# Kernel tuning notes

Measured on AMD Instinct MI355X. Metric: run time of the kernel, lower is better.

The kernel has to match this reference:

```python
import jax, jax.numpy as jnp
import numpy as np

B, S, H, A = 64, 200, 256, 16
CAPS_LAYERS = 3
NEG = -1e9
LN_EPS = 1e-12


def _layernorm(x, g, b):
    mu = jnp.mean(x, axis=-1, keepdims=True)
    var = jnp.mean(jnp.square(x - mu), axis=-1, keepdims=True)
    return (x - mu) / jnp.sqrt(var + LN_EPS) * g + b


def setup_inputs() -> dict:
    key = jax.random.key(0)
    ks = jax.random.split(key, 10)
    s = 0.02  # initializer_range
    return {
        "item_emb": jax.random.normal(ks[0], (B, S, H), jnp.float32),
        "item_seq": jax.random.randint(ks[1], (B, S), 0, 50000),
        "time_seq": jax.random.randint(ks[2], (B, S, 2), 0, 14),
        "W_lin": s * jax.random.normal(ks[3], (H, H), jnp.float32),
        "b_lin": jnp.zeros((H,), jnp.float32),
        "aspect_embs": s * jax.random.normal(ks[4], (A, H), jnp.float32),
        "pos_emb": s * jax.random.normal(ks[5], (S, H), jnp.float32),
        "tdt_emb": s * jax.random.normal(ks[6], (14, H), jnp.float32),
        "tdn_emb": s * jax.random.normal(ks[7], (14, H), jnp.float32),
        "Wa1": s * jax.random.normal(ks[8], (H, H), jnp.float32),
        "ba1": jnp.zeros((H,), jnp.float32),
        "Wa2": s * jax.random.normal(ks[9], (H,), jnp.float32),
        "ba2": jnp.zeros((1,), jnp.float32),
        "ln_g": jnp.ones((H,), jnp.float32),
        "ln_b": jnp.zeros((H,), jnp.float32),
    }


def reference(item_emb, item_seq, time_seq, W_lin, b_lin, aspect_embs,
              pos_emb, tdt_emb, tdn_emb, Wa1, ba1, Wa2, ba2, ln_g, ln_b):
    b, s = item_emb.shape[0], item_emb.shape[1]
    pad = item_seq == 0  # [B,S]

    # ---- TimeAwareAttention (seq_output has a singleton neighbor dim in torch) ----
    td = tdt_emb[time_seq[:, :, 0]] + tdn_emb[time_seq[:, :, 1]]       # [B,S,H]
    tma_in = pos_emb[None, :s] + item_emb + td                          # [B,S,H]
    h = tma_in @ Wa1 + ba1
    h = jnp.where(h >= 0, h, 0.01 * h)                                  # LeakyReLU
    w = h @ Wa2 + ba2[0]                                                # [B,S]
    w = jnp.where(pad, NEG, w)
    tma = jax.nn.softmax(w, axis=-1)                                    # [B,S]

    # ---- gating (eval: clean gates) ----
    gates = jnp.einsum('bsh,ah->bsa', item_emb, aspect_embs)            # [B,S,A]
    idx = jnp.argmax(gates, axis=-1)                                    # topk k=1, [B,S]

    src = jnp.where(pad, 0.0, 1.0)
    counts = jnp.zeros((b, A), jnp.float32).at[jnp.arange(b)[:, None], idx].add(src)
    aspect_mask = counts == 0                                           # [B,A]

    # ---- item transform (dropout = identity in eval) ----
    moe = _layernorm(jnp.tanh(item_emb @ W_lin + b_lin) + item_emb, ln_g, ln_b)  # [B,S,H]

    # ---- capsule routing ----
    bij = gates
    cap = jnp.broadcast_to(aspect_embs[None], (b, A, H))
    for _ in range(CAPS_LAYERS):
        cij = jnp.where(aspect_mask[:, None, :], NEG, bij)
        cij = jax.nn.softmax(cij, axis=-1)
        cij = jnp.where(pad[:, :, None], 0.0, cij)                      # [B,S,A]
        cap = jnp.einsum('bsa,bsh,bs->bah', cij, moe, tma)              # [B,A,H]
        n2 = jnp.sum(jnp.square(cap), axis=-1, keepdims=True)
        cap = n2 / (1.0 + n2) / jnp.sqrt(n2 + 1e-9) * cap               # squash
        bij = bij + jnp.einsum('bsh,bah->bsa', moe, cap)

    # ---- gather activated interests / activation positions ----
    activated = cap[jnp.arange(b)[:, None], idx]                        # [B,S,H]
    seq_pos = jnp.where(pad, 0, jnp.arange(1, s + 1)[None, :]).astype(jnp.float32)
    act_mat = jnp.full((b, s, A), -1.0, jnp.float32)
    act_mat = act_mat.at[jnp.arange(b)[:, None], jnp.arange(s)[None, :], idx].set(seq_pos)
    act_mat = jnp.where(pad[:, :, None], -1.0, act_mat)
    max_pos = jnp.max(act_mat, axis=1)                                  # [B,A]
    aspects_item_idx = jnp.where(max_pos > -1.0, max_pos - 1.0, max_pos)

    gates_sm = jax.nn.softmax(gates, axis=-1)
    return (cap, gates_sm, aspect_mask, activated, aspects_item_idx, idx[:, :, None])
```

## Files before the change

### kernel.cpp

```cpp
#include <hip/hip_runtime.h>

#define B_ 64
#define S_ 200
#define H_ 256
#define A_ 16
#define M_ (B_*S_)
#define NEGV (-1000000000.0f)

typedef unsigned short ushortT;
typedef __attribute__((ext_vector_type(8))) short short8;
typedef __attribute__((ext_vector_type(4))) float f32x4;

__device__ __forceinline__ ushortT bf16u(float f) {
  unsigned int u = __builtin_bit_cast(unsigned int, f);
  unsigned int r = (u + 0x7fffu + ((u >> 16) & 1u)) >> 16;
  return (ushortT)r;
}
__device__ __forceinline__ float bf2f(ushortT u) {
  unsigned int v = ((unsigned int)u) << 16;
  return __builtin_bit_cast(float, v);
}

__global__ __launch_bounds__(256) void prepT_kernel(
    const float* __restrict__ Wa1, const float* __restrict__ W_lin,
    ushortT* __restrict__ Wa1T, ushortT* __restrict__ WlinT)
{
  __shared__ float T[64*65];
  const int blk = blockIdx.x, t = threadIdx.x;
  int wsel = blk >> 4;
  int tile = blk & 15;
  const float* W = wsel ? W_lin : Wa1;
  ushortT* WT = wsel ? WlinT : Wa1T;
  int tr = (tile >> 2) * 64, tc = (tile & 3) * 64;
  #pragma unroll
  for (int p = 0; p < 16; ++p) {
    int r = p*4 + (t >> 6);
    int c = t & 63;
    T[c*65 + r] = W[(tr + r)*H_ + tc + c];
  }
  __syncthreads();
  #pragma unroll
  for (int p = 0; p < 16; ++p) {
    int n = p*4 + (t >> 6);
    int k = t & 63;
    WT[(tc + n)*H_ + tr + k] = bf16u(T[n*65 + k]);
  }
}

__global__ __launch_bounds__(512) void fused_kernel(
    const float* __restrict__ item, const int* __restrict__ iseq,
    const int* __restrict__ tseq, const float* __restrict__ pos,
    const float* __restrict__ tdt, const float* __restrict__ tdn,
    const float* __restrict__ asp,
    const ushortT* __restrict__ Wa1T, const ushortT* __restrict__ WlinT,
    const float* __restrict__ ba1, const float* __restrict__ Wa2,
    const float* __restrict__ ba2, const float* __restrict__ b_lin,
    const float* __restrict__ g_ln, const float* __restrict__ b_ln,
    float* __restrict__ w_out, ushortT* __restrict__ moe_outB,
    float* __restrict__ graw, float* __restrict__ gates_sm,
    float* __restrict__ idxf)
{
  __shared__ __align__(16) ushortT smem[51200];
  __shared__ int sL[64], ttL[64], tnL[64];
  __shared__ float wp[2][64], ln1[2][64], ln2[2][64], mus[64], rss[64];

  const int t = threadIdx.x;
  const int m0 = blockIdx.x * 64;
  const int lane = t & 63, w = t >> 6;
  const int g = w >> 2, wl = w & 3;
  const int wm = wl >> 1, wn = wl & 1;
  const int col = lane & 15;
  const int rg  = lane >> 4;

  if (t < 64) {
    int m = m0 + t;
    sL[t]  = m % S_;
    ttL[t] = tseq[2*m];
    tnL[t] = tseq[2*m+1];
  }
  __syncthreads();

  const int arow = t >> 3;
  const int ac4  = (t & 7) * 4;
  const int nr   = t >> 1;
  const int kh   = (t & 1) * 16;
  const int srow = sL[arow], trow = ttL[arow], nrow = tnL[arow];

  ushortT* const Atma0 = smem;
  ushortT* const Aitm0 = smem + 5120;
  ushortT* const B0b   = smem + 10240;
  ushortT* const B1b   = smem + 30720;

  float4 pi = *(const float4*)&item[(size_t)(m0+arow)*H_ + ac4];
  float4 pp = *(const float4*)&pos[srow*H_ + ac4];
  float4 pt = *(const float4*)&tdt[trow*H_ + ac4];
  float4 pn = *(const float4*)&tdn[nrow*H_ + ac4];
  uint4 b0a = *(const uint4*)&Wa1T[(size_t)nr*H_ + kh];
  uint4 b0b = *(const uint4*)&Wa1T[(size_t)nr*H_ + kh + 8];
  uint4 b1a = *(const uint4*)&WlinT[(size_t)nr*H_ + kh];
  uint4 b1b = *(const uint4*)&WlinT[(size_t)nr*H_ + kh + 8];
  {
    union { ushortT u[4]; uint2 v; } ci, ct;
    ci.u[0] = bf16u(pi.x); ci.u[1] = bf16u(pi.y);
    ci.u[2] = bf16u(pi.z); ci.u[3] = bf16u(pi.w);
    ct.u[0] = bf16u(pi.x + pp.x + pt.x + pn.x);
    ct.u[1] = bf16u(pi.y + pp.y + pt.y + pn.y);
    ct.u[2] = bf16u(pi.z + pp.z + pt.z + pn.z);
    ct.u[3] = bf16u(pi.w + pp.w + pt.w + pn.w);
    *(uint2*)&Aitm0[arow*40 + ac4] = ci.v;
    *(uint2*)&Atma0[arow*40 + ac4] = ct.v;
    *(uint4*)&B0b[nr*40 + kh]     = b0a;
    *(uint4*)&B0b[nr*40 + kh + 8] = b0b;
    *(uint4*)&B1b[nr*40 + kh]     = b1a;
    *(uint4*)&B1b[nr*40 + kh + 8] = b1b;
  }
  __syncthreads();

  f32x4 acc[2][8];
  #pragma unroll
  for (int r = 0; r < 2; ++r)
    #pragma unroll
    for (int q = 0; q < 8; ++q) acc[r][q] = (f32x4){0.f,0.f,0.f,0.f};

  #pragma unroll
  for (int ks = 0; ks < 8; ++ks) {
    if (ks < 7) {
      const int k1 = (ks + 1) * 32;
      pi = *(const float4*)&item[(size_t)(m0+arow)*H_ + k1 + ac4];
      pp = *(const float4*)&pos[srow*H_ + k1 + ac4];
      pt = *(const float4*)&tdt[trow*H_ + k1 + ac4];
      pn = *(const float4*)&tdn[nrow*H_ + k1 + ac4];
      b0a = *(const uint4*)&Wa1T[(size_t)nr*H_ + k1 + kh];
      b0b = *(const uint4*)&Wa1T[(size_t)nr*H_ + k1 + kh + 8];
      b1a = *(const uint4*)&WlinT[(size_t)nr*H_ + k1 + kh];
      b1b = *(const uint4*)&WlinT[(size_t)nr*H_ + k1 + kh + 8];
    }
    {
      const int p = ks & 1;
      const ushortT* Ab = (g ? Aitm0 : Atma0) + p*2560;
      const ushortT* Bb = (g ? B1b : B0b) + p*10240;
      short8 af0 = *(const short8*)&Ab[(wm*32 + col)*40 + rg*8];
      short8 af1 = *(const short8*)&Ab[(wm*32 + 16 + col)*40 + rg*8];
      #pragma unroll
      for (int q = 0; q < 8; ++q) {
        short8 bf = *(const short8*)&Bb[(wn*128 + q*16 + col)*40 + rg*8];
        acc[0][q] = __builtin_amdgcn_mfma_f32_16x16x32_bf16(af0, bf, acc[0][q], 0, 0, 0);
        acc[1][q] = __builtin_amdgcn_mfma_f32_16x16x32_bf16(af1, bf, acc[1][q], 0, 0, 0);
      }
    }
    if (ks < 7) {
      const int p = (ks + 1) & 1;
      union { ushortT u[4]; uint2 v; } ci, ct;
      ci.u[0] = bf16u(pi.x); ci.u[1] = bf16u(pi.y);
      ci.u[2] = bf16u(pi.z); ci.u[3] = bf16u(pi.w);
      ct.u[0] = bf16u(pi.x + pp.x + pt.x + pn.x);
      ct.u[1] = bf16u(pi.y + pp.y + pt.y + pn.y);
      ct.u[2] = bf16u(pi.z + pp.z + pt.z + pn.z);
      ct.u[3] = bf16u(pi.w + pp.w + pt.w + pn.w);
      *(uint2*)&(Aitm0 + p*2560)[arow*40 + ac4] = ci.v;
      *(uint2*)&(Atma0 + p*2560)[arow*40 + ac4] = ct.v;
      ushortT* B0w = B0b + p*10240;
      ushortT* B1w = B1b + p*10240;
      *(uint4*)&B0w[nr*40 + kh]     = b0a;
      *(uint4*)&B0w[nr*40 + kh + 8] = b0b;
      *(uint4*)&B1w[nr*40 + kh]     = b1a;
      *(uint4*)&B1w[nr*40 + kh + 8] = b1b;
    }
    __syncthreads();
  }

  float* aspl = (float*)smem;
  float* gL   = (float*)smem + 4160;
  #pragma unroll
  for (int i = 0; i < 2; ++i) {
    int e = t + 512*i;
    int r = e >> 6, c = e & 63;
    *(float4*)&aspl[r*260 + 4*c] = *(const float4*)&asp[r*H_ + 4*c];
  }

  float glv[8], bbv[8];
  if (g == 0) {
    float bav[8], wav[8];
    #pragma unroll
    for (int q = 0; q < 8; ++q) {
      int n = wn*128 + q*16 + col;
      bav[q] = ba1[n]; wav[q] = Wa2[n];
    }
    #pragma unroll
    for (int r = 0; r < 2; ++r)
      #pragma unroll
      for (int j = 0; j < 4; ++j) {
        float p = 0.f;
        #pragma unroll
        for (int q = 0; q < 8; ++q) {
          float h = acc[r][q][j] + bav[q];
          h = (h >= 0.f) ? h : 0.01f*h;
          p += h * wav[q];
        }
        #pragma unroll
        for (int mk = 1; mk < 16; mk <<= 1) p += __shfl_xor(p, mk);
        if (col == 0) wp[wn][wm*32 + r*16 + rg*4 + j] = p;
      }
  } else {
    float blv[8];
    #pragma unroll
    for (int q = 0; q < 8; ++q) {
      int n = wn*128 + q*16 + col;
      blv[q] = b_lin[n]; glv[q] = g_ln[n]; bbv[q] = b_ln[n];
    }
    #pragma unroll
    for (int r = 0; r < 2; ++r)
      #pragma unroll
      for (int j = 0; j < 4; ++j) {
        int row = wm*32 + r*16 + rg*4 + j;
        float s1 = 0.f, s2 = 0.f;
        #pragma unroll
        for (int q = 0; q < 8; ++q) {
          int n = wn*128 + q*16 + col;
          float vv = tanhf(acc[r][q][j] + blv[q]) + item[(size_t)(m0+row)*H_ + n];
          acc[r][q][j] = vv; s1 += vv; s2 += vv*vv;
        }
        #pragma unroll
        for (int mk = 1; mk < 16; mk <<= 1) {
          s1 += __shfl_xor(s1, mk);
          s2 += __shfl_xor(s2, mk);
        }
        if (col == 0) { ln1[wn][row] = s1; ln2[wn][row] = s2; }
      }
  }
  __syncthreads();
  if (t < 64) {
    int row = t, m = m0 + row;
    w_out[m] = (iseq[m] == 0) ? NEGV : (wp[0][row] + wp[1][row] + ba2[0]);
  } else if (t < 128) {
    int row = t - 64;
    float s1 = ln1[0][row] + ln1[1][row];
    float s2 = ln2[0][row] + ln2[1][row];
    float mu  = s1 * (1.0f/H_);
    float var = s2 * (1.0f/H_) - mu*mu;
    mus[row] = mu;
    rss[row] = 1.0f / sqrtf(fmaxf(var, 0.f) + 1e-12f);
  }
  __syncthreads();
  if (g == 1) {
    #pragma unroll
    for (int r = 0; r < 2; ++r)
      #pragma unroll
      for (int j = 0; j < 4; ++j) {
        int row = wm*32 + r*16 + rg*4 + j;
        int m = m0 + row;
        float mu = mus[row], rs = rss[row];
        #pragma unroll
        for (int q = 0; q < 8; ++q) {
          int n = wn*128 + q*16 + col;
          moe_outB[(size_t)m*H_ + n] = bf16u((acc[r][q][j] - mu)*rs*glv[q] + bbv[q]);
        }
      }
  }

  {
    const int r8 = t >> 3, a2 = (t & 7) * 2;
    const int m = m0 + r8;
    float ga = 0.f, gb = 0.f;
    #pragma unroll 8
    for (int k4 = 0; k4 < 64; ++k4) {
      float4 xv = *(const float4*)&item[(size_t)m*H_ + 4*k4];
      float4 a0 = *(const float4*)&aspl[a2*260 + 4*k4];
      float4 a1 = *(const float4*)&aspl[(a2+1)*260 + 4*k4];
      ga += xv.x*a0.x + xv.y*a0.y + xv.z*a0.z + xv.w*a0.w;
      gb += xv.x*a1.x + xv.y*a1.y + xv.z*a1.z + xv.w*a1.w;
    }
    gL[r8*20 + a2]     = ga;
    gL[r8*20 + a2 + 1] = gb;
  }
  __syncthreads();
  if (t < 64) {
    float row[16];
    #pragma unroll
    for (int a = 0; a < 16; ++a) row[a] = gL[t*20 + a];
    float best = row[0]; int bi = 0;
    #pragma unroll
    for (int a = 1; a < 16; ++a)
      if (row[a] > best) { best = row[a]; bi = a; }
    idxf[m0 + t] = (float)bi;
    float mx = row[0];
    #pragma unroll
    for (int a = 1; a < 16; ++a) mx = fmaxf(mx, row[a]);
    float ex[16], sm = 0.f;
    #pragma unroll
    for (int a = 0; a < 16; ++a) { ex[a] = expf(row[a] - mx); sm += ex[a]; }
    float inv = 1.f / sm;
    #pragma unroll
    for (int q = 0; q < 4; ++q) {
      float4 rv; rv.x = row[4*q]; rv.y = row[4*q+1]; rv.z = row[4*q+2]; rv.w = row[4*q+3];
      *(float4*)&graw[(m0+t)*A_ + 4*q] = rv;
      float4 o; o.x = ex[4*q]*inv; o.y = ex[4*q+1]*inv; o.z = ex[4*q+2]*inv; o.w = ex[4*q+3]*inv;
      *(float4*)&gates_sm[(m0+t)*A_ + 4*q] = o;
    }
  }
}

__device__ __forceinline__ float blk_max(float v, float* red) {
  #pragma unroll
  for (int mk = 32; mk; mk >>= 1) v = fmaxf(v, __shfl_xor(v, mk));
  int t = threadIdx.x;
  if ((t & 63) == 0) red[t >> 6] = v;
  __syncthreads();
  if (t < 64) {
    float x = (t < 16) ? red[t] : -3.0e38f;
    #pragma unroll
    for (int mk = 8; mk; mk >>= 1) x = fmaxf(x, __shfl_xor(x, mk));
    if (t == 0) red[0] = x;
  }
  __syncthreads();
  float r = red[0];
  __syncthreads();
  return r;
}

__device__ __forceinline__ float blk_sum(float v, float* red) {
  #pragma unroll
  for (int mk = 32; mk; mk >>= 1) v += __shfl_xor(v, mk);
  int t = threadIdx.x;
  if ((t & 63) == 0) red[t >> 6] = v;
  __syncthreads();
  if (t < 64) {
    float x = (t < 16) ? red[t] : 0.f;
    #pragma unroll
    for (int mk = 8; mk; mk >>= 1) x += __shfl_xor(x, mk);
    if (t == 0) red[0] = x;
  }
  __syncthreads();
  float r = red[0];
  __syncthreads();
  return r;
}

#define WGSTR 232
#define CBSTR 260
#define CLSTR 252

__global__ __launch_bounds__(1024) void phaseC_kernel(
    const int* __restrict__ iseq, const float* __restrict__ w_in,
    const ushortT* __restrict__ moeB, const float* __restrict__ idxf,
    const float* __restrict__ graw,
    float* __restrict__ cap_out,
    float* __restrict__ mask_out,
    float* __restrict__ aidx_out,
    float* __restrict__ act_out)
{
  __shared__ ushortT moeTr[57344];
  __shared__ ushortT wgtT[16*WGSTR];
  __shared__ ushortT capB[16*CBSTR];
  __shared__ float bij[4032];
  __shared__ float n2p[16*17];
  __shared__ float n2s[16];
  __shared__ float tmaL[S_];
  __shared__ float red[16];
  __shared__ float maskf[A_];
  __shared__ int counts[A_], maxpos[A_];
  __shared__ int idxl[S_];
  __shared__ int padl[S_];

  const int t = threadIdx.x;
  const int b = blockIdx.x;
  const int base = b * S_;
  const int lane = t & 63, w = t >> 6;
  const int la = lane & 15, lg = lane >> 4;

  #pragma unroll
  for (int u = 0; u < 4; ++u) {
    int e = t + 1024*u;
    if (e < 3584) {
      int ht = e & 15, s = e >> 4;
      int ks = s >> 5, s4l = (s >> 2) & 7, sr = s & 3;
      int bp = (s4l & 1) ? 4 + (s4l >> 1) : (s4l >> 1);
      int li = ((ht*7 + ks)*8 + bp)*64 + sr*16;
      if (s < S_) {
        const ushortT* gp = &moeB[((size_t)(base + s))*H_ + ht*16];
        *(uint4*)&moeTr[li]     = *(const uint4*)gp;
        *(uint4*)&moeTr[li + 8] = *(const uint4*)(gp + 8);
      } else {
        uint4 z = {0,0,0,0};
        *(uint4*)&moeTr[li] = z; *(uint4*)&moeTr[li + 8] = z;
      }
    }
  }
  if (t < 512) {
    int a = t >> 5, s = 200 + (t & 31);
    wgtT[a*WGSTR + s] = 0;
  }

  if (t < A_) { counts[t] = 0; maxpos[t] = -1; }
  float wv = -3.0e38f;
  if (t < S_) {
    int s = t;
    padl[s] = (iseq[base+s] == 0) ? 1 : 0;
    idxl[s] = (int)idxf[base+s];
    wv = w_in[base+s];
    #pragma unroll
    for (int q = 0; q < 4; ++q)
      *(float4*)&bij[s*20 + 4*q] = *(const float4*)&graw[(base+s)*A_ + 4*q];
  }
  __syncthreads();

  short8 a2[7];
  {
    unsigned vA = (unsigned)(w*7168 + lane*8);
    #pragma unroll
    for (int ks = 0; ks < 7; ++ks) {
      long long r0, r1;
      asm volatile(
        "ds_read_b64_tr_b16 %0, %2\n\t"
        "ds_read_b64_tr_b16 %1, %2 offset:512\n\t"
        "s_waitcnt lgkmcnt(0)"
        : "=&v"(r0), "=&v"(r1) : "v"(vA + (unsigned)(ks*1024)) : "memory");
      __builtin_amdgcn_sched_barrier(0);
      union { short8 v; long long q[2]; } uu;
      uu.q[0] = r0; uu.q[1] = r1;
      a2[ks] = uu.v;
    }
  }

  if (t < S_ && !padl[t]) {
    atomicAdd(&counts[idxl[t]], 1);
    atomicMax(&maxpos[idxl[t]], t + 1);
  }
  float mxw = blk_max(wv, red);
  float ev = (t < S_) ? expf(wv - mxw) : 0.f;
  float sw = blk_sum(ev, red);
  if (t < S_) tmaL[t] = ev / sw;
  __syncthreads();
  if (t < A_) {
    int c = counts[t];
    float mkv = (c == 0) ? 1.f : 0.f;
    maskf[t] = mkv;
    mask_out[b*A_ + t] = mkv;
    int mp = maxpos[t];
    aidx_out[b*A_ + t] = (mp > 0) ? (float)(mp - 1) : -1.f;
  }
  __syncthreads();

  for (int iter = 0; iter < 3; ++iter) {
    #pragma unroll
    for (int pass = 0; pass < 4; ++pass) {
      int s = pass*64 + (t >> 4);
      int a = t & 15;
      if (s < S_) {
        float v = bij[s*20 + a];
        v = (maskf[a] > 0.5f) ? NEGV : v;
        float mx = v;
        #pragma unroll
        for (int mk = 1; mk < 16; mk <<= 1) mx = fmaxf(mx, __shfl_xor(mx, mk));
        float e = expf(v - mx);
        float sm = e;
        #pragma unroll
        for (int mk = 1; mk < 16; mk <<= 1) sm += __shfl_xor(sm, mk);
        float sc = (padl[s] ? 0.f : tmaL[s]) / sm;
        wgtT[a*WGSTR + s] = bf16u(e*sc);
      }
    }
    __syncthreads();

    f32x4 acc = (f32x4){0.f,0.f,0.f,0.f};
    #pragma unroll
    for (int ks = 0; ks < 7; ++ks) {
      short8 bf = *(const short8*)&wgtT[la*WGSTR + ks*32 + lg*8];
      acc = __builtin_amdgcn_mfma_f32_16x16x32_bf16(a2[ks], bf, acc, 0, 0, 0);
    }
    {
      float n2 = acc[0]*acc[0] + acc[1]*acc[1] + acc[2]*acc[2] + acc[3]*acc[3];
      n2 += __shfl_xor(n2, 16);
      n2 += __shfl_xor(n2, 32);
      if (lane < 16) n2p[w*17 + lane] = n2;
    }
    __syncthreads();
    if (t < 16) {
      float sv = 0.f;
      #pragma unroll
      for (int w2 = 0; w2 < 16; ++w2) sv += n2p[w2*17 + t];
      n2s[t] = sv / (1.f + sv) / sqrtf(sv + 1e-9f);
    }
    __syncthreads();
    {
      float sc = n2s[la];
      if (iter < 2) {
        #pragma unroll
        for (int r = 0; r < 4; ++r)
          capB[la*CBSTR + w*16 + lg*4 + r] = bf16u(acc[r]*sc);
      } else {
        float* capl = bij;
        #pragma unroll
        for (int r = 0; r < 4; ++r)
          capl[la*CLSTR + w*16 + lg*4 + r] = acc[r]*sc;
      }
    }
    __syncthreads();

    if (iter < 2) {
      if (w < 13) {
        int sR = w*16 + la;
        int ksS = sR >> 5, s4l = (sR >> 2) & 7, sr = sR & 3;
        int bp = (s4l & 1) ? 4 + (s4l >> 1) : (s4l >> 1);
        int laneA = ksS*512 + bp*64 + sr*16 + (lg & 1)*8 + (lg >> 1)*3584;
        f32x4 accS = (f32x4){0.f,0.f,0.f,0.f};
        #pragma unroll
        for (int k4 = 0; k4 < 8; ++k4) {
          short8 am = *(const short8*)&moeTr[laneA + k4*7168];
          short8 bc = *(const short8*)&capB[la*CBSTR + k4*32 + lg*8];
          accS = __builtin_amdgcn_mfma_f32_16x16x32_bf16(am, bc, accS, 0, 0, 0);
        }
        int sW = w*16 + lg*4;
        #pragma unroll
        for (int r = 0; r < 4; ++r)
          if (sW + r < S_) bij[(sW + r)*20 + la] += accS[r];
      }
      __syncthreads();
    }
  }

  {
    const float* capl = bij;
    int a = t >> 6, h4 = t & 63;
    float4 v = *(const float4*)&capl[a*CLSTR + 4*h4];
    *(float4*)&cap_out[((size_t)b*A_ + a)*H_ + 4*h4] = v;
    for (int s = t >> 6; s < S_; s += 16) {
      float4 av = *(const float4*)&capl[idxl[s]*CLSTR + 4*h4];
      *(float4*)&act_out[((size_t)base + s)*H_ + 4*h4] = av;
    }
  }
}

extern "C" void kernel_launch(void* const* d_in, const int* in_sizes, int n_in,
                              void* d_out, int out_size, void* d_ws, size_t ws_size,
                              hipStream_t stream) {
  (void)in_sizes; (void)n_in; (void)out_size; (void)ws_size;
  const float* item  = (const float*)d_in[0];
  const int*   iseq  = (const int*)d_in[1];
  const int*   tseq  = (const int*)d_in[2];
  const float* W_lin = (const float*)d_in[3];
  const float* b_lin = (const float*)d_in[4];
  const float* asp   = (const float*)d_in[5];
  const float* pos   = (const float*)d_in[6];
  const float* tdt   = (const float*)d_in[7];
  const float* tdn   = (const float*)d_in[8];
  const float* Wa1   = (const float*)d_in[9];
  const float* ba1   = (const float*)d_in[10];
  const float* Wa2   = (const float*)d_in[11];
  const float* ba2   = (const float*)d_in[12];
  const float* g_ln  = (const float*)d_in[13];
  const float* b_ln  = (const float*)d_in[14];

  float* out    = (float*)d_out;
  float* cap_o  = out;
  float* gate_o = out + 262144;
  float* mask_o = out + 466944;
  float* act_o  = out + 467968;
  float* aidx_o = out + 3744768;
  float* idx_o  = out + 3745792;

  ushortT* moeB  = (ushortT*)d_ws;
  ushortT* Wa1T  = (ushortT*)((char*)d_ws + 6553600);
  ushortT* WlinT = (ushortT*)((char*)d_ws + 6553600 + 131072);
  float*   w_ws  = (float*)((char*)d_ws + 6553600 + 262144);
  float*   graw  = (float*)((char*)d_ws + 6553600 + 262144 + 51200);

  prepT_kernel<<<32, 256, 0, stream>>>(Wa1, W_lin, Wa1T, WlinT);
  fused_kernel<<<200, 512, 0, stream>>>(item, iseq, tseq, pos, tdt, tdn, asp,
      Wa1T, WlinT, ba1, Wa2, ba2, b_lin, g_ln, b_ln, w_ws, moeB,
      graw, gate_o, idx_o);
  phaseC_kernel<<<B_, 1024, 0, stream>>>(iseq, w_ws, moeB, idx_o, graw,
      cap_o, mask_o, aidx_o, act_o);
}
```

Before: 57.95 us.

## Move activated-interest gather into separate wide kernel and remap gate dot products

The write of the activated-interest tensor (B*S*H floats) moves out of the 64-block phaseC kernel into a new gather kernel with many blocks, each thread copying one float4 from cap by the stored argmax index. The goal is to spread this large write across the whole GPU instead of only 64 workgroups. The gate dot-product loop is also remapped so each thread handles one aspect for two rows, sharing each aspect-vector load between two rows. The price is an extra kernel launch and rereading cap and idx from global memory.

```diff
diff --git a/kernel.cpp b/kernel.cpp
--- a/kernel.cpp
+++ b/kernel.cpp
@@ -259,19 +259,21 @@
   }
 
   {
-    const int r8 = t >> 3, a2 = (t & 7) * 2;
-    const int m = m0 + r8;
+    const int a  = t & 15;
+    const int r2 = (t >> 4) * 2;
     float ga = 0.f, gb = 0.f;
+    const float* x0p = &item[(size_t)(m0 + r2)*H_];
+    const float* x1p = &item[(size_t)(m0 + r2 + 1)*H_];
     #pragma unroll 8
     for (int k4 = 0; k4 < 64; ++k4) {
-      float4 xv = *(const float4*)&item[(size_t)m*H_ + 4*k4];
-      float4 a0 = *(const float4*)&aspl[a2*260 + 4*k4];
-      float4 a1 = *(const float4*)&aspl[(a2+1)*260 + 4*k4];
-      ga += xv.x*a0.x + xv.y*a0.y + xv.z*a0.z + xv.w*a0.w;
-      gb += xv.x*a1.x + xv.y*a1.y + xv.z*a1.z + xv.w*a1.w;
-    }
-    gL[r8*20 + a2]     = ga;
-    gL[r8*20 + a2 + 1] = gb;
+      float4 av = *(const float4*)&aspl[a*260 + 4*k4];
+      float4 x0 = *(const float4*)&x0p[4*k4];
+      float4 x1 = *(const float4*)&x1p[4*k4];
+      ga += x0.x*av.x + x0.y*av.y + x0.z*av.z + x0.w*av.w;
+      gb += x1.x*av.x + x1.y*av.y + x1.z*av.z + x1.w*av.w;
+    }
+    gL[r2*20 + a]       = ga;
+    gL[(r2 + 1)*20 + a] = gb;
   }
   __syncthreads();
   if (t < 64) {
@@ -346,8 +348,7 @@
     const float* __restrict__ graw,
     float* __restrict__ cap_out,
     float* __restrict__ mask_out,
-    float* __restrict__ aidx_out,
-    float* __restrict__ act_out)
+    float* __restrict__ aidx_out)
 {
   __shared__ ushortT moeTr[57344];
   __shared__ ushortT wgtT[16*WGSTR];
@@ -524,11 +525,19 @@
     int a = t >> 6, h4 = t & 63;
     float4 v = *(const float4*)&capl[a*CLSTR + 4*h4];
     *(float4*)&cap_out[((size_t)b*A_ + a)*H_ + 4*h4] = v;
-    for (int s = t >> 6; s < S_; s += 16) {
-      float4 av = *(const float4*)&capl[idxl[s]*CLSTR + 4*h4];
-      *(float4*)&act_out[((size_t)base + s)*H_ + 4*h4] = av;
-    }
-  }
+  }
+}
+
+__global__ __launch_bounds__(256) void gather_kernel(
+    const float* __restrict__ capv, const float* __restrict__ idxf,
+    float* __restrict__ act)
+{
+  int e4 = blockIdx.x * 256 + threadIdx.x;
+  int m = e4 >> 6, h4 = e4 & 63;
+  int b = m / S_;
+  int id = (int)idxf[m];
+  float4 v = *(const float4*)&capv[((b*A_) + id)*H_ + 4*h4];
+  *(float4*)&act[(size_t)4*e4] = v;
 }
 
 extern "C" void kernel_launch(void* const* d_in, const int* in_sizes, int n_in,
@@ -570,5 +579,6 @@
       Wa1T, WlinT, ba1, Wa2, ba2, b_lin, g_ln, b_ln, w_ws, moeB,
       graw, gate_o, idx_o);
   phaseC_kernel<<<B_, 1024, 0, stream>>>(iseq, w_ws, moeB, idx_o, graw,
-      cap_o, mask_o, aidx_o, act_o);
-}
+      cap_o, mask_o, aidx_o);
+  gather_kernel<<<(M_*H_/4)/256, 256, 0, stream>>>(cap_o, idx_o, act_o);
+}
```

Result: slower. 62.73 us (+8.3%).
